# Kernel optimization log

Measured on AMD Instinct MI355X. Metric: run time of the kernel, lower is better.

The kernel has to match this reference:

```python
import jax, jax.numpy as jnp
import numpy as np
import math

NUM_HEADS = 32
NUM_KV_HEADS = 8
HEAD_DIM = 128
HIDDEN = 4096
BATCH = 2
SEQ = 2048
MASK_MIN = -1e9


def _rope(x, cos, sin):
    # x: [B, S, H, D], cos/sin: [S, D/2]
    d2 = x.shape[-1] // 2
    x1, x2 = x[..., :d2], x[..., d2:]
    c = cos[None, :, None, :]
    s = sin[None, :, None, :]
    return jnp.concatenate([x1 * c - x2 * s, x2 * c + x1 * s], axis=-1)


def setup_inputs() -> dict:
    key = jax.random.key(0)
    k1, k2, k3 = jax.random.split(key, 3)
    hidden_states = jax.random.normal(k1, (BATCH, SEQ, HIDDEN), dtype=jnp.float32) * 0.02
    Wqkv = jax.random.normal(k2, (HIDDEN, (NUM_HEADS + 2 * NUM_KV_HEADS) * HEAD_DIM), dtype=jnp.float32) * (HIDDEN ** -0.5)
    Wo = jax.random.normal(k3, (NUM_HEADS * HEAD_DIM, HIDDEN), dtype=jnp.float32) * (HIDDEN ** -0.5)
    pos = np.arange(SEQ, dtype=np.float32)
    inv_freq = 1.0 / (10000.0 ** (np.arange(0, HEAD_DIM, 2, dtype=np.float32) / HEAD_DIM))
    freqs = np.outer(pos, inv_freq)  # [S, D/2]
    cos = jnp.asarray(np.cos(freqs), dtype=jnp.float32)
    sin = jnp.asarray(np.sin(freqs), dtype=jnp.float32)
    # causal additive mask [B, 1, S, S]
    causal = np.triu(np.full((SEQ, SEQ), MASK_MIN, dtype=np.float32), k=1)
    attention_mask = jnp.broadcast_to(jnp.asarray(causal)[None, None], (BATCH, 1, SEQ, SEQ))
    return {"hidden_states": hidden_states, "Wqkv": Wqkv, "Wo": Wo,
            "cos": cos, "sin": sin, "attention_mask": attention_mask}


def reference(hidden_states, Wqkv, Wo, cos, sin, attention_mask):
    B, S, H = hidden_states.shape
    n_rep = NUM_HEADS // NUM_KV_HEADS
    qkv = jnp.einsum('bsh,hd->bsd', hidden_states, Wqkv)
    q_end = NUM_HEADS * HEAD_DIM
    k_end = q_end + NUM_KV_HEADS * HEAD_DIM
    q = qkv[..., :q_end].reshape(B, S, NUM_HEADS, HEAD_DIM)
    k = qkv[..., q_end:k_end].reshape(B, S, NUM_KV_HEADS, HEAD_DIM)
    v = qkv[..., k_end:].reshape(B, S, NUM_KV_HEADS, HEAD_DIM)
    q = _rope(q, cos, sin)
    k = _rope(k, cos, sin)
    # repeat_kv: expand kv heads to query heads
    k = jnp.repeat(k, n_rep, axis=2)  # [B, S, NH, D]
    v = jnp.repeat(v, n_rep, axis=2)
    scores = jnp.einsum('bqhd,bkhd->bhqk', q, k) / math.sqrt(HEAD_DIM)
    scores = scores + attention_mask
    scores = jnp.maximum(scores, jnp.finfo(scores.dtype).min)
    probs = jax.nn.softmax(scores.astype(jnp.float32), axis=-1).astype(q.dtype)
    attn = jnp.einsum('bhqk,bkhd->bqhd', probs, v)  # [B, S, NH, D]
    attn = attn.reshape(B, S, NUM_HEADS * HEAD_DIM)
    return jnp.einsum('bsd,dh->bsh', attn, Wo)
```

## Files before the change

### kernel.cpp

```cpp
#include <hip/hip_runtime.h>

typedef unsigned short u16;
typedef __bf16 bf16x8 __attribute__((ext_vector_type(8)));
typedef float f32x4 __attribute__((ext_vector_type(4)));
typedef float f32x16 __attribute__((ext_vector_type(16)));
typedef u16 u16x4 __attribute__((ext_vector_type(4)));

#define SEQ 2048
#define NQKV 6144
#define HID 4096

__device__ inline u16 f2bf(float f) {
  union { float f; unsigned u; } x; x.f = f;
  unsigned r = x.u + 0x7fffu + ((x.u >> 16) & 1u);
  return (u16)(r >> 16);
}
__device__ inline float bf2f(u16 u) {
  union { unsigned u; float f; } x; x.u = ((unsigned)u) << 16;
  return x.f;
}
__device__ inline f32x4 mfma16(bf16x8 a, bf16x8 b, f32x4 c) {
  return __builtin_amdgcn_mfma_f32_16x16x32_bf16(a, b, c, 0, 0, 0);
}
__device__ inline f32x16 mfma32(bf16x8 a, bf16x8 b, f32x16 c) {
  return __builtin_amdgcn_mfma_f32_32x32x16_bf16(a, b, c, 0, 0, 0);
}
__device__ inline unsigned cvtpk(float lo, float hi) {
  unsigned r;
  asm("v_cvt_pk_bf16_f32 %0, %1, %2" : "=v"(r) : "v"(lo), "v"(hi));
  return r;
}
__device__ inline void gload16(const void* g, void* l) {
  __builtin_amdgcn_global_load_lds((const __attribute__((address_space(1))) void*)g,
                                   (__attribute__((address_space(3))) void*)l,
                                   16, 0, 0);
}

__global__ __launch_bounds__(256) void conv_kernel(const float* __restrict__ in,
                                                   u16* __restrict__ out) {
  int i = (blockIdx.x * 256 + threadIdx.x) * 4;
  float4 v = *(const float4*)(in + i);
  u16x4 o;
  o[0] = f2bf(v.x); o[1] = f2bf(v.y); o[2] = f2bf(v.z); o[3] = f2bf(v.w);
  *(u16x4*)(out + i) = o;
}

__global__ __launch_bounds__(256) void transconv_kernel(const float* __restrict__ in,
                                                        u16* __restrict__ out,
                                                        int R, int C) {
  __shared__ u16 tile[32][33];
  int c0 = blockIdx.x * 32, r0 = blockIdx.y * 32;
  int tx = threadIdx.x & 31, ty = threadIdx.x >> 5;
  for (int i = 0; i < 4; ++i)
    tile[ty + 8 * i][tx] = f2bf(in[(size_t)(r0 + ty + 8 * i) * C + c0 + tx]);
  __syncthreads();
  for (int i = 0; i < 4; ++i)
    out[(size_t)(c0 + ty + 8 * i) * R + r0 + tx] = tile[tx][ty + 8 * i];
}

__device__ inline void store_out(u16* p, float v) { *p = f2bf(v); }
__device__ inline void store_out(float* p, float v) { *p = v; }

template <typename OutT>
__global__ __launch_bounds__(512, 2) void gemm_kernel(const u16* __restrict__ A,
                                                      const u16* __restrict__ Bt,
                                                      OutT* __restrict__ C,
                                                      int M, int N, int K, int nby) {
  __shared__ __align__(16) u16 As[2][256 * 64];
  __shared__ __align__(16) u16 Bs[2][256 * 64];
  int nwg = gridDim.x;
  int bid = blockIdx.x;
  int s = (bid & 7) * (nwg >> 3) + (bid >> 3);
  int by = s % nby, bx = s / nby;
  int row0 = by * 256, col0 = bx * 256;
  int tid = threadIdx.x, w = tid >> 6, l = tid & 63;
  int wm = w >> 2, wn = w & 3;
  int lo = l & 15, hi = l >> 4;
  int lr = l >> 3;
  int lc = (l & 7) ^ ((l >> 3) & 7);
  const u16* Ab = A + (size_t)row0 * K;
  const u16* Bb = Bt + (size_t)col0 * K;
  int nkt = K >> 6;

  f32x4 acc[8][4] = {};

#define STAGE(tt, g)                                                          \
  { int ci = (g) * 8 + w;                                                     \
    gload16(Ab + (size_t)(ci * 8 + lr) * K + (tt) * 64 + lc * 8,              \
            &As[(tt) & 1][ci * 512]);                                         \
    gload16(Bb + (size_t)(ci * 8 + lr) * K + (tt) * 64 + lc * 8,              \
            &Bs[(tt) & 1][ci * 512]); }
#define RD_A(cur, qm, fm, kh, dst)                                            \
  { int r = wm * 128 + (qm) * 64 + (fm) * 16 + lo;                            \
    dst = *(const bf16x8*)&As[cur][r * 64 + ((((kh) * 4 + hi) ^ (r & 7)) * 8)]; }
#define RD_B(cur, qn, fn, kh, dst)                                            \
  { int r = wn * 64 + (qn) * 32 + (fn) * 16 + lo;                             \
    dst = *(const bf16x8*)&Bs[cur][r * 64 + ((((kh) * 4 + hi) ^ (r & 7)) * 8)]; }

  STAGE(0, 0); STAGE(0, 1); STAGE(0, 2); STAGE(0, 3);
  asm volatile("s_waitcnt vmcnt(0)" ::: "memory");
  __builtin_amdgcn_s_barrier();

  bf16x8 af[4][2], bfr[2][2];
  for (int t = 0; t < nkt; ++t) {
    int cur = t & 1;
    bool pf = (t + 1 < nkt);
    for (int fm = 0; fm < 4; ++fm)
      for (int kh = 0; kh < 2; ++kh) RD_A(cur, 0, fm, kh, af[fm][kh]);
    for (int fn = 0; fn < 2; ++fn)
      for (int kh = 0; kh < 2; ++kh) RD_B(cur, 0, fn, kh, bfr[fn][kh]);
    if (pf) { STAGE(t + 1, 0); STAGE(t + 1, 1); }
    __builtin_amdgcn_s_barrier();
    __builtin_amdgcn_s_setprio(1);
    for (int fm = 0; fm < 4; ++fm)
      for (int fn = 0; fn < 2; ++fn)
        for (int kh = 0; kh < 2; ++kh)
          acc[fm][fn] = mfma16(af[fm][kh], bfr[fn][kh], acc[fm][fn]);
    __builtin_amdgcn_s_setprio(0);
    for (int fm = 0; fm < 4; ++fm)
      for (int kh = 0; kh < 2; ++kh) RD_A(cur, 1, fm, kh, af[fm][kh]);
    if (pf) STAGE(t + 1, 2);
    __builtin_amdgcn_s_barrier();
    __builtin_amdgcn_s_setprio(1);
    for (int fm = 0; fm < 4; ++fm)
      for (int fn = 0; fn < 2; ++fn)
        for (int kh = 0; kh < 2; ++kh)
          acc[4 + fm][fn] = mfma16(af[fm][kh], bfr[fn][kh], acc[4 + fm][fn]);
    __builtin_amdgcn_s_setprio(0);
    for (int fn = 0; fn < 2; ++fn)
      for (int kh = 0; kh < 2; ++kh) RD_B(cur, 1, fn, kh, bfr[fn][kh]);
    if (pf) STAGE(t + 1, 3);
    __builtin_amdgcn_s_barrier();
    __builtin_amdgcn_s_setprio(1);
    for (int fm = 0; fm < 4; ++fm)
      for (int fn = 0; fn < 2; ++fn)
        for (int kh = 0; kh < 2; ++kh)
          acc[4 + fm][2 + fn] = mfma16(af[fm][kh], bfr[fn][kh], acc[4 + fm][2 + fn]);
    __builtin_amdgcn_s_setprio(0);
    for (int fm = 0; fm < 4; ++fm)
      for (int kh = 0; kh < 2; ++kh) RD_A(cur, 0, fm, kh, af[fm][kh]);
    __builtin_amdgcn_s_barrier();
    __builtin_amdgcn_s_setprio(1);
    for (int fm = 0; fm < 4; ++fm)
      for (int fn = 0; fn < 2; ++fn)
        for (int kh = 0; kh < 2; ++kh)
          acc[fm][2 + fn] = mfma16(af[fm][kh], bfr[fn][kh], acc[fm][2 + fn]);
    __builtin_amdgcn_s_setprio(0);
    asm volatile("s_waitcnt vmcnt(0)" ::: "memory");
    __builtin_amdgcn_s_barrier();
  }
#undef STAGE
#undef RD_A
#undef RD_B

  for (int im = 0; im < 8; ++im)
    for (int in = 0; in < 4; ++in)
      for (int rr = 0; rr < 4; ++rr) {
        int row = row0 + wm * 128 + im * 16 + hi * 4 + rr;
        int col = col0 + wn * 64 + in * 16 + lo;
        store_out(&C[(size_t)row * N + col], acc[im][in][rr]);
      }
}

__global__ __launch_bounds__(256) void rope_kernel(u16* __restrict__ qkv,
                                                   const float* __restrict__ cosb,
                                                   const float* __restrict__ sinb) {
  int idx = blockIdx.x * 256 + threadIdx.x;
  int d = idx & 63;
  int head = (idx >> 6) % 40;
  int m = idx / (64 * 40);
  int s = m & (SEQ - 1);
  int col = head < 32 ? head * 128 : 4096 + (head - 32) * 128;
  u16* p = qkv + (size_t)m * NQKV + col;
  float x1 = bf2f(p[d]), x2 = bf2f(p[d + 64]);
  float c = cosb[s * 64 + d], sn = sinb[s * 64 + d];
  p[d] = f2bf(x1 * c - x2 * sn);
  p[d + 64] = f2bf(x2 * c + x1 * sn);
}

__global__ __launch_bounds__(256) void vtrans_kernel(const u16* __restrict__ qkv,
                                                     u16* __restrict__ Vt) {
  __shared__ u16 tile[32][33];
  int bid = blockIdx.x;
  int dt = bid & 3;
  int st = (bid >> 2) & 63;
  int bk = bid >> 8;
  int b = bk >> 3, kvh = bk & 7;
  int tx = threadIdx.x & 31, ty = threadIdx.x >> 5;
  for (int i = 0; i < 4; ++i) {
    int s = st * 32 + ty + 8 * i;
    tile[ty + 8 * i][tx] = qkv[(size_t)(b * SEQ + s) * NQKV + 5120 + kvh * 128 + dt * 32 + tx];
  }
  __syncthreads();
  for (int i = 0; i < 4; ++i) {
    int d = dt * 32 + ty + 8 * i;
    Vt[((size_t)bk * 128 + d) * SEQ + st * 32 + tx] = tile[tx][ty + 8 * i];
  }
}

__global__ __launch_bounds__(256, 2) void flash_kernel(const u16* __restrict__ qkv,
                                                       const u16* __restrict__ Vt,
                                                       u16* __restrict__ attn) {
  const float C2 = 0.12751740f;
  int bid = blockIdx.x;
  int bh = bid & 63;
  int pr = bid >> 6;
  int h = bh & 31;
  int b = bh >> 5;
  int w = threadIdx.x >> 6, l = threadIdx.x & 63;
  int hv = l >> 5;
  int q32 = l & 31;
  int kvh = h >> 2;

  __shared__ __align__(16) u16 Ks[2][64 * 128];
  __shared__ __align__(16) u16 Vs[2][128 * 64];

  const u16* kb = qkv + (size_t)(b * SEQ) * NQKV + 4096 + kvh * 128;
  const u16* vtb = Vt + (size_t)(b * 8 + kvh) * 128 * SEQ;

#define STAGEKV(TT, BF)                                                       \
  { _Pragma("unroll")                                                         \
    for (int i = 0; i < 4; ++i) {                                             \
      int ck = w * 4 + i;                                                     \
      int rk = ck * 4 + (l >> 4);                                             \
      gload16(kb + (size_t)((TT) * 64 + rk) * NQKV + (((l & 15) ^ (rk & 7)) * 8), \
              &Ks[BF][ck * 512]);                                             \
      int rv = ck * 8 + (l >> 3);                                             \
      gload16(vtb + (size_t)rv * SEQ + (TT) * 64 + (((l & 7) ^ (rv & 7)) * 8), \
              &Vs[BF][ck * 512]);                                             \
    } }

  for (int pass = 0; pass < 2; ++pass) {
    int qc = pass ? 15 - pr : pr;
    int q0 = qc * 128 + w * 32;
    int qg = q0 + q32;
    __syncthreads();

    bf16x8 qf[8];
    {
      const u16* qr = qkv + (size_t)(b * SEQ + qg) * NQKV + h * 128 + hv * 8;
#pragma unroll
      for (int d0 = 0; d0 < 8; ++d0) qf[d0] = *(const bf16x8*)(qr + d0 * 16);
    }
    f32x16 o[4] = {};
    float mreg = -1e30f, lreg = 0.f;
    int ktend = 2 * qc + 1;
    int mykt = 2 * qc + (w >> 1);

    STAGEKV(0, 0);
    for (int kt = 0; kt <= ktend; ++kt) {
      int buf = kt & 1;
      if (kt < ktend) {
        STAGEKV(kt + 1, buf ^ 1);
        asm volatile("s_waitcnt vmcnt(8)" ::: "memory");
      } else {
        asm volatile("s_waitcnt vmcnt(0)" ::: "memory");
      }
      __builtin_amdgcn_s_barrier();

      if (kt <= mykt) {
        f32x16 s0 = {}, s1 = {};
        int swzk = q32 & 7;
#pragma unroll
        for (int d0 = 0; d0 < 8; ++d0) {
          int sl = (((d0 * 2 + hv) ^ swzk) * 8);
          bf16x8 k0 = *(const bf16x8*)&Ks[buf][q32 * 128 + sl];
          bf16x8 k1 = *(const bf16x8*)&Ks[buf][(32 + q32) * 128 + sl];
          s0 = mfma32(k0, qf[d0], s0);
          s1 = mfma32(k1, qf[d0], s1);
        }
        if (kt == mykt) {
#pragma unroll
          for (int r = 0; r < 16; ++r) {
            int kloc = (r & 3) + 8 * (r >> 2) + 4 * hv;
            if (kt * 64 + kloc > qg) s0[r] = -1e30f;
            if (kt * 64 + 32 + kloc > qg) s1[r] = -1e30f;
          }
        }
        float pm = -1e30f;
#pragma unroll
        for (int r = 0; r < 16; ++r) {
          pm = fmaxf(pm, s0[r]);
          pm = fmaxf(pm, s1[r]);
        }
        pm = fmaxf(pm, __shfl_xor(pm, 32));
        if (!__all(pm - mreg <= 62.746f)) {
          float mnew = fmaxf(mreg, pm);
          float al = exp2f((mreg - mnew) * C2);
          lreg *= al;
#pragma unroll
          for (int r = 0; r < 16; ++r) {
            o[0][r] *= al; o[1][r] *= al; o[2][r] *= al; o[3][r] *= al;
          }
          mreg = mnew;
        }
        float rs = 0.f;
#pragma unroll
        for (int r = 0; r < 16; ++r) {
          s0[r] = exp2f((s0[r] - mreg) * C2); rs += s0[r];
          s1[r] = exp2f((s1[r] - mreg) * C2); rs += s1[r];
        }
        rs += __shfl_xor(rs, 32);
        lreg += rs;
        bf16x8 pa[4];
#define MKPA(KSI, SP, RB)                                                     \
        { unsigned wA = cvtpk(SP[(RB) + 0], SP[(RB) + 1]);                    \
          unsigned wB = cvtpk(SP[(RB) + 2], SP[(RB) + 3]);                    \
          unsigned wC = cvtpk(SP[(RB) + 4], SP[(RB) + 5]);                    \
          unsigned wD = cvtpk(SP[(RB) + 6], SP[(RB) + 7]);                    \
          unsigned sA = __shfl_xor(wA, 32), sB = __shfl_xor(wB, 32);          \
          unsigned sC = __shfl_xor(wC, 32), sD = __shfl_xor(wD, 32);          \
          union { unsigned u[4]; bf16x8 v; } pk;                              \
          pk.u[0] = hv ? sC : wA; pk.u[1] = hv ? sD : wB;                     \
          pk.u[2] = hv ? wC : sA; pk.u[3] = hv ? wD : sB;                     \
          pa[KSI] = pk.v; }
        MKPA(0, s0, 0) MKPA(1, s0, 8) MKPA(2, s1, 0) MKPA(3, s1, 8)
#undef MKPA
#pragma unroll
        for (int db = 0; db < 4; ++db) {
          int rv = db * 32 + q32;
          int swz = rv & 7;
#pragma unroll
          for (int ks = 0; ks < 4; ++ks) {
            bf16x8 vf = *(const bf16x8*)&Vs[buf][rv * 64 + (((ks * 2 + hv) ^ swz) * 8)];
            o[db] = mfma32(vf, pa[ks], o[db]);
          }
        }
      }
    }
    float invl = 1.0f / lreg;
    u16* op = attn + (size_t)(b * SEQ + qg) * 4096 + h * 128 + hv * 4;
#pragma unroll
    for (int db = 0; db < 4; ++db)
#pragma unroll
      for (int g = 0; g < 4; ++g) {
        unsigned w0 = cvtpk(o[db][g * 4 + 0] * invl, o[db][g * 4 + 1] * invl);
        unsigned w1 = cvtpk(o[db][g * 4 + 2] * invl, o[db][g * 4 + 3] * invl);
        uint2 val; val.x = w0; val.y = w1;
        *(uint2*)(op + db * 32 + g * 8) = val;
      }
  }
#undef STAGEKV
}

extern "C" void kernel_launch(void* const* d_in, const int* in_sizes, int n_in,
                              void* d_out, int out_size, void* d_ws, size_t ws_size,
                              hipStream_t stream) {
  const float* hidden = (const float*)d_in[0];
  const float* Wqkv = (const float*)d_in[1];
  const float* Wo = (const float*)d_in[2];
  const float* cosb = (const float*)d_in[3];
  const float* sinb = (const float*)d_in[4];
  float* out = (float*)d_out;

  char* ws = (char*)d_ws;
  u16* R1 = (u16*)ws;
  u16* R2 = (u16*)(ws + 50331648);
  u16* R3 = (u16*)(ws + 100663296);

  conv_kernel<<<16384, 256, 0, stream>>>(hidden, R3);
  transconv_kernel<<<dim3(6144 / 32, 4096 / 32), 256, 0, stream>>>(Wqkv, R1, 4096, 6144);
  gemm_kernel<u16><<<384, 512, 0, stream>>>(R3, R1, R2, 4096, 6144, 4096, 16);
  rope_kernel<<<40960, 256, 0, stream>>>(R2, cosb, sinb);
  vtrans_kernel<<<4096, 256, 0, stream>>>(R2, R3);
  flash_kernel<<<512, 256, 0, stream>>>(R2, R3, R1);
  transconv_kernel<<<dim3(4096 / 32, 4096 / 32), 256, 0, stream>>>(Wo, R2, 4096, 4096);
  gemm_kernel<float><<<256, 512, 0, stream>>>(R1, R2, out, 4096, 4096, 4096, 16);
}
```

Measured before the change: 545.0 us.

## Restructure GEMM into templated tiles with 4-stage K=32 software pipeline

Rewrites the GEMM kernel so the tile shape is a template parameter. The K step shrinks from 64 to 32 and the double buffer becomes a 4-slot LDS ring that prefetches three tiles ahead, with partial vmcnt waits in place of a full drain every iteration. The QKV projection now uses 128x384 tiles over 512 blocks, while the output projection keeps 256x256. The goal is to hide global-load latency better and balance the QKV grid across CUs, at the cost of more barriers per unit of K and a changed LDS swizzle.

```diff
diff --git a/kernel.cpp b/kernel.cpp
--- a/kernel.cpp
+++ b/kernel.cpp
@@ -61,104 +61,105 @@
 __device__ inline void store_out(u16* p, float v) { *p = f2bf(v); }
 __device__ inline void store_out(float* p, float v) { *p = v; }
 
-template <typename OutT>
+template <int MF, int NF, typename OutT>
 __global__ __launch_bounds__(512, 2) void gemm_kernel(const u16* __restrict__ A,
                                                       const u16* __restrict__ Bt,
                                                       OutT* __restrict__ C,
                                                       int M, int N, int K, int nby) {
-  __shared__ __align__(16) u16 As[2][256 * 64];
-  __shared__ __align__(16) u16 Bs[2][256 * 64];
+  constexpr int BM = 32 * MF;
+  constexpr int BN = 64 * NF;
+  __shared__ __align__(16) u16 As[4][BM * 32];
+  __shared__ __align__(16) u16 Bs[4][BN * 32];
   int nwg = gridDim.x;
   int bid = blockIdx.x;
   int s = (bid & 7) * (nwg >> 3) + (bid >> 3);
   int by = s % nby, bx = s / nby;
-  int row0 = by * 256, col0 = bx * 256;
+  int row0 = by * BM, col0 = bx * BN;
   int tid = threadIdx.x, w = tid >> 6, l = tid & 63;
   int wm = w >> 2, wn = w & 3;
   int lo = l & 15, hi = l >> 4;
-  int lr = l >> 3;
-  int lc = (l & 7) ^ ((l >> 3) & 7);
+  int sr = tid >> 2;
+  int lc = (tid & 3) ^ ((tid >> 3) & 3);
   const u16* Ab = A + (size_t)row0 * K;
   const u16* Bb = Bt + (size_t)col0 * K;
-  int nkt = K >> 6;
-
-  f32x4 acc[8][4] = {};
-
-#define STAGE(tt, g)                                                          \
-  { int ci = (g) * 8 + w;                                                     \
-    gload16(Ab + (size_t)(ci * 8 + lr) * K + (tt) * 64 + lc * 8,              \
-            &As[(tt) & 1][ci * 512]);                                         \
-    gload16(Bb + (size_t)(ci * 8 + lr) * K + (tt) * 64 + lc * 8,              \
-            &Bs[(tt) & 1][ci * 512]); }
-#define RD_A(cur, qm, fm, kh, dst)                                            \
-  { int r = wm * 128 + (qm) * 64 + (fm) * 16 + lo;                            \
-    dst = *(const bf16x8*)&As[cur][r * 64 + ((((kh) * 4 + hi) ^ (r & 7)) * 8)]; }
-#define RD_B(cur, qn, fn, kh, dst)                                            \
-  { int r = wn * 64 + (qn) * 32 + (fn) * 16 + lo;                             \
-    dst = *(const bf16x8*)&Bs[cur][r * 64 + ((((kh) * 4 + hi) ^ (r & 7)) * 8)]; }
-
-  STAGE(0, 0); STAGE(0, 1); STAGE(0, 2); STAGE(0, 3);
-  asm volatile("s_waitcnt vmcnt(0)" ::: "memory");
+  int nkt = K >> 5;
+
+  f32x4 acc[MF][NF] = {};
+
+#define STAGE_A(tt)                                                           \
+  { _Pragma("unroll")                                                         \
+    for (int j = 0; j < BM / 128; ++j) {                                      \
+      int row = j * 128 + sr;                                                 \
+      gload16(Ab + (size_t)row * K + (tt) * 32 + lc * 8,                      \
+              &As[(tt) & 3][row * 32 + (tid & 3) * 8]);                       \
+    } }
+#define STAGE_B(tt)                                                           \
+  { _Pragma("unroll")                                                         \
+    for (int j = 0; j < BN / 128; ++j) {                                      \
+      int row = j * 128 + sr;                                                 \
+      gload16(Bb + (size_t)row * K + (tt) * 32 + lc * 8,                      \
+              &Bs[(tt) & 3][row * 32 + (tid & 3) * 8]);                       \
+    } }
+#define RD_A(cur, fm, dst)                                                    \
+  { int r = wm * 16 * MF + (fm) * 16 + lo;                                    \
+    dst = *(const bf16x8*)&As[cur][r * 32 + ((hi ^ ((r >> 1) & 3)) * 8)]; }
+#define RD_B(cur, fn, dst)                                                    \
+  { int r = wn * 16 * NF + (fn) * 16 + lo;                                    \
+    dst = *(const bf16x8*)&Bs[cur][r * 32 + ((hi ^ ((r >> 1) & 3)) * 8)]; }
+
+  for (int tt = 0; tt < 3; ++tt) { STAGE_A(tt); STAGE_B(tt); }
+  asm volatile("s_waitcnt vmcnt(8)" ::: "memory");
   __builtin_amdgcn_s_barrier();
 
-  bf16x8 af[4][2], bfr[2][2];
+  bf16x8 af[MF], bfr[NF / 2];
   for (int t = 0; t < nkt; ++t) {
-    int cur = t & 1;
-    bool pf = (t + 1 < nkt);
-    for (int fm = 0; fm < 4; ++fm)
-      for (int kh = 0; kh < 2; ++kh) RD_A(cur, 0, fm, kh, af[fm][kh]);
-    for (int fn = 0; fn < 2; ++fn)
-      for (int kh = 0; kh < 2; ++kh) RD_B(cur, 0, fn, kh, bfr[fn][kh]);
-    if (pf) { STAGE(t + 1, 0); STAGE(t + 1, 1); }
+    int cur = t & 3;
+    bool pf = (t + 3 < nkt);
+#pragma unroll
+    for (int fm = 0; fm < MF; ++fm) RD_A(cur, fm, af[fm]);
+#pragma unroll
+    for (int fn = 0; fn < NF / 2; ++fn) RD_B(cur, fn, bfr[fn]);
+    if (pf) STAGE_A(t + 3);
     __builtin_amdgcn_s_barrier();
     __builtin_amdgcn_s_setprio(1);
-    for (int fm = 0; fm < 4; ++fm)
-      for (int fn = 0; fn < 2; ++fn)
-        for (int kh = 0; kh < 2; ++kh)
-          acc[fm][fn] = mfma16(af[fm][kh], bfr[fn][kh], acc[fm][fn]);
+#pragma unroll
+    for (int fm = 0; fm < MF; ++fm)
+#pragma unroll
+      for (int fn = 0; fn < NF / 2; ++fn)
+        acc[fm][fn] = mfma16(af[fm], bfr[fn], acc[fm][fn]);
     __builtin_amdgcn_s_setprio(0);
-    for (int fm = 0; fm < 4; ++fm)
-      for (int kh = 0; kh < 2; ++kh) RD_A(cur, 1, fm, kh, af[fm][kh]);
-    if (pf) STAGE(t + 1, 2);
+    __builtin_amdgcn_s_barrier();
+#pragma unroll
+    for (int fn = 0; fn < NF / 2; ++fn) RD_B(cur, NF / 2 + fn, bfr[fn]);
+    if (pf) STAGE_B(t + 3);
+    if (t + 3 < nkt) {
+      asm volatile("s_waitcnt vmcnt(8)" ::: "memory");
+    } else if (t + 2 < nkt) {
+      asm volatile("s_waitcnt vmcnt(4)" ::: "memory");
+    } else {
+      asm volatile("s_waitcnt vmcnt(0)" ::: "memory");
+    }
     __builtin_amdgcn_s_barrier();
     __builtin_amdgcn_s_setprio(1);
-    for (int fm = 0; fm < 4; ++fm)
-      for (int fn = 0; fn < 2; ++fn)
-        for (int kh = 0; kh < 2; ++kh)
-          acc[4 + fm][fn] = mfma16(af[fm][kh], bfr[fn][kh], acc[4 + fm][fn]);
+#pragma unroll
+    for (int fm = 0; fm < MF; ++fm)
+#pragma unroll
+      for (int fn = 0; fn < NF / 2; ++fn)
+        acc[fm][NF / 2 + fn] = mfma16(af[fm], bfr[fn], acc[fm][NF / 2 + fn]);
     __builtin_amdgcn_s_setprio(0);
-    for (int fn = 0; fn < 2; ++fn)
-      for (int kh = 0; kh < 2; ++kh) RD_B(cur, 1, fn, kh, bfr[fn][kh]);
-    if (pf) STAGE(t + 1, 3);
-    __builtin_amdgcn_s_barrier();
-    __builtin_amdgcn_s_setprio(1);
-    for (int fm = 0; fm < 4; ++fm)
-      for (int fn = 0; fn < 2; ++fn)
-        for (int kh = 0; kh < 2; ++kh)
-          acc[4 + fm][2 + fn] = mfma16(af[fm][kh], bfr[fn][kh], acc[4 + fm][2 + fn]);
-    __builtin_amdgcn_s_setprio(0);
-    for (int fm = 0; fm < 4; ++fm)
-      for (int kh = 0; kh < 2; ++kh) RD_A(cur, 0, fm, kh, af[fm][kh]);
-    __builtin_amdgcn_s_barrier();
-    __builtin_amdgcn_s_setprio(1);
-    for (int fm = 0; fm < 4; ++fm)
-      for (int fn = 0; fn < 2; ++fn)
-        for (int kh = 0; kh < 2; ++kh)
-          acc[fm][2 + fn] = mfma16(af[fm][kh], bfr[fn][kh], acc[fm][2 + fn]);
-    __builtin_amdgcn_s_setprio(0);
-    asm volatile("s_waitcnt vmcnt(0)" ::: "memory");
     __builtin_amdgcn_s_barrier();
   }
-#undef STAGE
+#undef STAGE_A
+#undef STAGE_B
 #undef RD_A
 #undef RD_B
 
-  for (int im = 0; im < 8; ++im)
-    for (int in = 0; in < 4; ++in)
+  for (int fm = 0; fm < MF; ++fm)
+    for (int fn = 0; fn < NF; ++fn)
       for (int rr = 0; rr < 4; ++rr) {
-        int row = row0 + wm * 128 + im * 16 + hi * 4 + rr;
-        int col = col0 + wn * 64 + in * 16 + lo;
-        store_out(&C[(size_t)row * N + col], acc[im][in][rr]);
+        int row = row0 + wm * 16 * MF + fm * 16 + hi * 4 + rr;
+        int col = col0 + wn * 16 * NF + fn * 16 + lo;
+        store_out(&C[(size_t)row * N + col], acc[fm][fn][rr]);
       }
 }
 
@@ -360,10 +361,10 @@
 
   conv_kernel<<<16384, 256, 0, stream>>>(hidden, R3);
   transconv_kernel<<<dim3(6144 / 32, 4096 / 32), 256, 0, stream>>>(Wqkv, R1, 4096, 6144);
-  gemm_kernel<u16><<<384, 512, 0, stream>>>(R3, R1, R2, 4096, 6144, 4096, 16);
+  gemm_kernel<4, 6, u16><<<512, 512, 0, stream>>>(R3, R1, R2, 4096, 6144, 4096, 32);
   rope_kernel<<<40960, 256, 0, stream>>>(R2, cosb, sinb);
   vtrans_kernel<<<4096, 256, 0, stream>>>(R2, R3);
   flash_kernel<<<512, 256, 0, stream>>>(R2, R3, R1);
   transconv_kernel<<<dim3(4096 / 32, 4096 / 32), 256, 0, stream>>>(Wo, R2, 4096, 4096);
-  gemm_kernel<float><<<256, 512, 0, stream>>>(R1, R2, out, 4096, 4096, 4096, 16);
-}
+  gemm_kernel<8, 4, float><<<256, 512, 0, stream>>>(R1, R2, out, 4096, 4096, 4096, 16);
+}
```

New measurement: 575.7 us. 5.6% more time.

## Split GEMM LDS tiles into K-halves with finer-grained prefetch and waitcnt pipelining

Applied to the files above, without the earlier changes.

The GEMM's shared-memory tiles are split into two 32-wide K halves per buffer, using a new 4-chunk XOR swizzle, and loaded per half with separate A and B stages. The main loop is restructured into four MFMA phases over K-halves and M-halves, with partial vmcnt waits so the next half's global loads stay in flight while the current half is consumed. This aims to overlap global loads with compute more tightly and cut full-drain stalls. In exchange it adds more barriers per iteration, and the changed swizzle could alter LDS bank conflicts.

```diff
diff --git a/kernel.cpp b/kernel.cpp
--- a/kernel.cpp
+++ b/kernel.cpp
@@ -66,8 +66,8 @@
                                                       const u16* __restrict__ Bt,
                                                       OutT* __restrict__ C,
                                                       int M, int N, int K, int nby) {
-  __shared__ __align__(16) u16 As[2][256 * 64];
-  __shared__ __align__(16) u16 Bs[2][256 * 64];
+  __shared__ __align__(16) u16 As[2][2][256 * 32];
+  __shared__ __align__(16) u16 Bs[2][2][256 * 32];
   int nwg = gridDim.x;
   int bid = blockIdx.x;
   int s = (bid & 7) * (nwg >> 3) + (bid >> 3);
@@ -76,89 +76,109 @@
   int tid = threadIdx.x, w = tid >> 6, l = tid & 63;
   int wm = w >> 2, wn = w & 3;
   int lo = l & 15, hi = l >> 4;
-  int lr = l >> 3;
-  int lc = (l & 7) ^ ((l >> 3) & 7);
+  int sr = tid >> 2;
+  int sc = tid & 3;
+  int lc = sc ^ ((tid >> 3) & 3);
   const u16* Ab = A + (size_t)row0 * K;
   const u16* Bb = Bt + (size_t)col0 * K;
   int nkt = K >> 6;
 
   f32x4 acc[8][4] = {};
 
-#define STAGE(tt, g)                                                          \
-  { int ci = (g) * 8 + w;                                                     \
-    gload16(Ab + (size_t)(ci * 8 + lr) * K + (tt) * 64 + lc * 8,              \
-            &As[(tt) & 1][ci * 512]);                                         \
-    gload16(Bb + (size_t)(ci * 8 + lr) * K + (tt) * 64 + lc * 8,              \
-            &Bs[(tt) & 1][ci * 512]); }
-#define RD_A(cur, qm, fm, kh, dst)                                            \
-  { int r = wm * 128 + (qm) * 64 + (fm) * 16 + lo;                            \
-    dst = *(const bf16x8*)&As[cur][r * 64 + ((((kh) * 4 + hi) ^ (r & 7)) * 8)]; }
-#define RD_B(cur, qn, fn, kh, dst)                                            \
-  { int r = wn * 64 + (qn) * 32 + (fn) * 16 + lo;                             \
-    dst = *(const bf16x8*)&Bs[cur][r * 64 + ((((kh) * 4 + hi) ^ (r & 7)) * 8)]; }
-
-  STAGE(0, 0); STAGE(0, 1); STAGE(0, 2); STAGE(0, 3);
-  asm volatile("s_waitcnt vmcnt(0)" ::: "memory");
+#define STA(tt, kh)                                                           \
+  { _Pragma("unroll")                                                         \
+    for (int j = 0; j < 2; ++j) {                                             \
+      int row = j * 128 + sr;                                                 \
+      gload16(Ab + (size_t)row * K + (tt) * 64 + (kh) * 32 + lc * 8,          \
+              &As[(tt) & 1][kh][row * 32 + sc * 8]);                          \
+    } }
+#define STB(tt, kh)                                                           \
+  { _Pragma("unroll")                                                         \
+    for (int j = 0; j < 2; ++j) {                                             \
+      int row = j * 128 + sr;                                                 \
+      gload16(Bb + (size_t)row * K + (tt) * 64 + (kh) * 32 + lc * 8,          \
+              &Bs[(tt) & 1][kh][row * 32 + sc * 8]);                          \
+    } }
+#define RA(cur, kh, fm, dst)                                                  \
+  { int r = wm * 128 + (fm) * 16 + lo;                                        \
+    dst = *(const bf16x8*)&As[cur][kh][r * 32 + ((hi ^ ((r >> 1) & 3)) * 8)]; }
+#define RB(cur, kh, fn, dst)                                                  \
+  { int r = wn * 64 + (fn) * 16 + lo;                                         \
+    dst = *(const bf16x8*)&Bs[cur][kh][r * 32 + ((hi ^ ((r >> 1) & 3)) * 8)]; }
+
+  STA(0, 0); STB(0, 0); STA(0, 1); STB(0, 1);
+  asm volatile("s_waitcnt vmcnt(4)" ::: "memory");
   __builtin_amdgcn_s_barrier();
 
-  bf16x8 af[4][2], bfr[2][2];
+  bf16x8 af[4], bfr[4];
   for (int t = 0; t < nkt; ++t) {
     int cur = t & 1;
     bool pf = (t + 1 < nkt);
+    RA(cur, 0, 0, af[0]); RA(cur, 0, 1, af[1]); RA(cur, 0, 2, af[2]); RA(cur, 0, 3, af[3]);
+    RB(cur, 0, 0, bfr[0]); RB(cur, 0, 1, bfr[1]); RB(cur, 0, 2, bfr[2]); RB(cur, 0, 3, bfr[3]);
+    if (pf) STA(t + 1, 0);
+    __builtin_amdgcn_s_barrier();
+    asm volatile("s_waitcnt lgkmcnt(0)" ::: "memory");
+    __builtin_amdgcn_s_setprio(1);
+#pragma unroll
     for (int fm = 0; fm < 4; ++fm)
-      for (int kh = 0; kh < 2; ++kh) RD_A(cur, 0, fm, kh, af[fm][kh]);
-    for (int fn = 0; fn < 2; ++fn)
-      for (int kh = 0; kh < 2; ++kh) RD_B(cur, 0, fn, kh, bfr[fn][kh]);
-    if (pf) { STAGE(t + 1, 0); STAGE(t + 1, 1); }
-    __builtin_amdgcn_s_barrier();
+#pragma unroll
+      for (int fn = 0; fn < 4; ++fn)
+        acc[fm][fn] = mfma16(af[fm], bfr[fn], acc[fm][fn]);
+    __builtin_amdgcn_s_setprio(0);
+    __builtin_amdgcn_s_barrier();
+    RA(cur, 0, 4, af[0]); RA(cur, 0, 5, af[1]); RA(cur, 0, 6, af[2]); RA(cur, 0, 7, af[3]);
+    if (pf) STB(t + 1, 0);
+    __builtin_amdgcn_s_barrier();
+    asm volatile("s_waitcnt lgkmcnt(0)" ::: "memory");
     __builtin_amdgcn_s_setprio(1);
+#pragma unroll
     for (int fm = 0; fm < 4; ++fm)
-      for (int fn = 0; fn < 2; ++fn)
-        for (int kh = 0; kh < 2; ++kh)
-          acc[fm][fn] = mfma16(af[fm][kh], bfr[fn][kh], acc[fm][fn]);
+#pragma unroll
+      for (int fn = 0; fn < 4; ++fn)
+        acc[4 + fm][fn] = mfma16(af[fm], bfr[fn], acc[4 + fm][fn]);
     __builtin_amdgcn_s_setprio(0);
+    if (pf) { asm volatile("s_waitcnt vmcnt(4)" ::: "memory"); }
+    else    { asm volatile("s_waitcnt vmcnt(0)" ::: "memory"); }
+    __builtin_amdgcn_s_barrier();
+    RA(cur, 1, 0, af[0]); RA(cur, 1, 1, af[1]); RA(cur, 1, 2, af[2]); RA(cur, 1, 3, af[3]);
+    RB(cur, 1, 0, bfr[0]); RB(cur, 1, 1, bfr[1]); RB(cur, 1, 2, bfr[2]); RB(cur, 1, 3, bfr[3]);
+    if (pf) STA(t + 1, 1);
+    __builtin_amdgcn_s_barrier();
+    asm volatile("s_waitcnt lgkmcnt(0)" ::: "memory");
+    __builtin_amdgcn_s_setprio(1);
+#pragma unroll
     for (int fm = 0; fm < 4; ++fm)
-      for (int kh = 0; kh < 2; ++kh) RD_A(cur, 1, fm, kh, af[fm][kh]);
-    if (pf) STAGE(t + 1, 2);
-    __builtin_amdgcn_s_barrier();
+#pragma unroll
+      for (int fn = 0; fn < 4; ++fn)
+        acc[fm][fn] = mfma16(af[fm], bfr[fn], acc[fm][fn]);
+    __builtin_amdgcn_s_setprio(0);
+    __builtin_amdgcn_s_barrier();
+    RA(cur, 1, 4, af[0]); RA(cur, 1, 5, af[1]); RA(cur, 1, 6, af[2]); RA(cur, 1, 7, af[3]);
+    if (pf) STB(t + 1, 1);
+    __builtin_amdgcn_s_barrier();
+    asm volatile("s_waitcnt lgkmcnt(0)" ::: "memory");
     __builtin_amdgcn_s_setprio(1);
+#pragma unroll
     for (int fm = 0; fm < 4; ++fm)
-      for (int fn = 0; fn < 2; ++fn)
-        for (int kh = 0; kh < 2; ++kh)
-          acc[4 + fm][fn] = mfma16(af[fm][kh], bfr[fn][kh], acc[4 + fm][fn]);
+#pragma unroll
+      for (int fn = 0; fn < 4; ++fn)
+        acc[4 + fm][fn] = mfma16(af[fm], bfr[fn], acc[4 + fm][fn]);
     __builtin_amdgcn_s_setprio(0);
-    for (int fn = 0; fn < 2; ++fn)
-      for (int kh = 0; kh < 2; ++kh) RD_B(cur, 1, fn, kh, bfr[fn][kh]);
-    if (pf) STAGE(t + 1, 3);
-    __builtin_amdgcn_s_barrier();
-    __builtin_amdgcn_s_setprio(1);
-    for (int fm = 0; fm < 4; ++fm)
-      for (int fn = 0; fn < 2; ++fn)
-        for (int kh = 0; kh < 2; ++kh)
-          acc[4 + fm][2 + fn] = mfma16(af[fm][kh], bfr[fn][kh], acc[4 + fm][2 + fn]);
-    __builtin_amdgcn_s_setprio(0);
-    for (int fm = 0; fm < 4; ++fm)
-      for (int kh = 0; kh < 2; ++kh) RD_A(cur, 0, fm, kh, af[fm][kh]);
-    __builtin_amdgcn_s_barrier();
-    __builtin_amdgcn_s_setprio(1);
-    for (int fm = 0; fm < 4; ++fm)
-      for (int fn = 0; fn < 2; ++fn)
-        for (int kh = 0; kh < 2; ++kh)
-          acc[fm][2 + fn] = mfma16(af[fm][kh], bfr[fn][kh], acc[fm][2 + fn]);
-    __builtin_amdgcn_s_setprio(0);
-    asm volatile("s_waitcnt vmcnt(0)" ::: "memory");
+    if (pf) { asm volatile("s_waitcnt vmcnt(4)" ::: "memory"); }
     __builtin_amdgcn_s_barrier();
   }
-#undef STAGE
-#undef RD_A
-#undef RD_B
-
-  for (int im = 0; im < 8; ++im)
-    for (int in = 0; in < 4; ++in)
+#undef STA
+#undef STB
+#undef RA
+#undef RB
+
+  for (int fm = 0; fm < 8; ++fm)
+    for (int fn = 0; fn < 4; ++fn)
       for (int rr = 0; rr < 4; ++rr) {
-        int row = row0 + wm * 128 + im * 16 + hi * 4 + rr;
-        int col = col0 + wn * 64 + in * 16 + lo;
-        store_out(&C[(size_t)row * N + col], acc[im][in][rr]);
+        int row = row0 + wm * 128 + fm * 16 + hi * 4 + rr;
+        int col = col0 + wn * 64 + fn * 16 + lo;
+        store_out(&C[(size_t)row * N + col], acc[fm][fn][rr]);
       }
 }
 
```

Result: no change. 553.2 us (+1.5%).
